# Kernel optimization log

Hardware: AMD Instinct MI355X
Metric: run time of the kernel (lower is better)

Reference implementation:

```python
import jax, jax.numpy as jnp
import numpy as np
from jax import lax

B, N, C = 8, 2000, 81            # batch, proposals, classes
MAX_INST = 100                    # config.detection_max_instances
MIN_CONF = 0.05                   # config.detection_min_confidence
NMS_THR = 0.3                     # config.detection_nms_threshold
H, W = 512, 512                   # config.image_shape[:2]
CLASS_OFFSET = 2.0                # > window extent, separates classes for batched NMS


def setup_inputs() -> dict:
    key = jax.random.key(0)
    k1, k2, k3, k4 = jax.random.split(key, 4)
    # valid normalized boxes (y1<y2, x1<x2)
    ctr = jax.random.uniform(k1, (B, N, 2))
    sz = jax.random.uniform(k2, (B, N, 2), minval=0.02, maxval=0.25)
    lo = jnp.clip(ctr - sz / 2, 0.0, 1.0)
    hi = jnp.clip(ctr + sz / 2, 0.0, 1.0)
    rois = jnp.stack([lo[..., 0], lo[..., 1], hi[..., 0], hi[..., 1]], axis=-1)
    probs = jax.nn.softmax(4.0 * jax.random.normal(k3, (B, N, C)), axis=-1)
    deltas = 0.1 * jax.random.normal(k4, (B, N, C, 4))
    bbox_std_dev = jnp.array([0.1, 0.1, 0.2, 0.2], jnp.float32)
    return {"rois": rois, "probs": probs, "deltas": deltas,
            "bbox_std_dev": bbox_std_dev}


def _apply_box_deltas(boxes, d):
    # boxes [N,4] (y1,x1,y2,x2), d [N,4] (dy,dx,log dh,log dw)
    h = boxes[:, 2] - boxes[:, 0]
    w = boxes[:, 3] - boxes[:, 1]
    cy = boxes[:, 0] + 0.5 * h + d[:, 0] * h
    cx = boxes[:, 1] + 0.5 * w + d[:, 1] * w
    h = h * jnp.exp(d[:, 2])
    w = w * jnp.exp(d[:, 3])
    return jnp.stack([cy - 0.5 * h, cx - 0.5 * w, cy + 0.5 * h, cx + 0.5 * w], axis=1)


def _pairwise_iou(b):
    # b [N,4] -> [N,N]
    area = (b[:, 2] - b[:, 0]) * (b[:, 3] - b[:, 1])
    yy1 = jnp.maximum(b[:, None, 0], b[None, :, 0])
    xx1 = jnp.maximum(b[:, None, 1], b[None, :, 1])
    yy2 = jnp.minimum(b[:, None, 2], b[None, :, 2])
    xx2 = jnp.minimum(b[:, None, 3], b[None, :, 3])
    inter = jnp.maximum(yy2 - yy1, 0.0) * jnp.maximum(xx2 - xx1, 0.0)
    union = area[:, None] + area[None, :] - inter
    return inter / jnp.maximum(union, 1e-12)


def _refine_one(rois, probs, deltas, bbox_std_dev):
    # rois [N,4], probs [N,C], deltas [N,C,4]
    cls = jnp.argmax(probs, axis=1)                       # [N] int
    idx = jnp.arange(N)
    scores = probs[idx, cls]                              # [N]
    d = deltas[idx, cls] * bbox_std_dev                   # [N,4]
    refined = jnp.clip(_apply_box_deltas(rois, d), 0.0, 1.0)  # window (0,0,1,1)
    valid = (cls > 0) & (scores >= MIN_CONF)
    # sort by score desc; invalid last
    order = jnp.argsort(-jnp.where(valid, scores, -jnp.inf))
    b = refined[order]
    s = scores[order]
    c = cls[order]
    v = valid[order]
    # per-class NMS via class-offset trick (equivalent to per-class NMS)
    ob = b + CLASS_OFFSET * c[:, None].astype(b.dtype)
    iou = _pairwise_iou(ob)                               # [N,N]

    def body(i, carry):
        keep, counts = carry
        sup = jnp.any(keep & (iou[i] > NMS_THR))
        ci = c[i]
        ok = v[i] & (~sup) & (counts[ci] < MAX_INST)      # per-class max_output_size
        return keep.at[i].set(ok), counts.at[ci].add(ok.astype(jnp.int32))

    keep, _ = lax.fori_loop(0, N, body,
                            (jnp.zeros((N,), bool), jnp.zeros((C,), jnp.int32)))
    kscores = jnp.where(keep, s, -jnp.inf)
    topv, topi = lax.top_k(kscores, MAX_INST)             # global top-k, sorted
    dvalid = topv > -jnp.inf
    boxes = jnp.where(dvalid[:, None], b[topi], 0.0)
    cls_f = jnp.where(dvalid, c[topi].astype(jnp.float32), 0.0)
    scr = jnp.where(dvalid, topv, 0.0)
    return jnp.concatenate([boxes, cls_f[:, None], scr[:, None]], axis=1)  # [MAX_INST,6]


def _attention_mask(det):
    # det [B,MAX_INST,6]; padded rows are all-zero boxes -> cover no pixels
    ys = (jnp.arange(H, dtype=jnp.float32) + 0.5) / H
    xs = (jnp.arange(W, dtype=jnp.float32) + 0.5) / W
    iny = (ys >= det[:, :, 0:1]) & (ys < det[:, :, 2:3])  # [B,D,H]
    inx = (xs >= det[:, :, 1:2]) & (xs < det[:, :, 3:4])  # [B,D,W]
    m = jnp.einsum('bdh,bdw->bhw', iny.astype(jnp.float32), inx.astype(jnp.float32))
    return (m > 0).astype(jnp.float32)


def reference(rois, probs, deltas, bbox_std_dev):
    det = jax.vmap(lambda r, p, dl: _refine_one(r, p, dl, bbox_std_dev))(rois, probs, deltas)
    mask = _attention_mask(det)
    return det, mask
```

## Files before the change

### kernel.cpp

```cpp
#include <hip/hip_runtime.h>
#include <math.h>

#define BB 8
#define NN 2000
#define CC 81
#define NPAD 2048
#define MAXI 100
#define HH 512
#define WW 512

__global__ void k_refine(const float* __restrict__ rois,
                         const float* __restrict__ probs,
                         const float* __restrict__ deltas,
                         const float* __restrict__ stdv,
                         float* __restrict__ score, int* __restrict__ cls,
                         int* __restrict__ valid, float* __restrict__ box,
                         unsigned long long* __restrict__ gkeys) {
#pragma clang fp contract(off)
  int g = blockIdx.x * 4 + (threadIdx.x >> 6);
  if (g >= BB * NPAD) return;
  int lane = threadIdx.x & 63;
  int b = g >> 11, n = g & (NPAD - 1);
  if (n >= NN) {
    if (lane == 0) {
      unsigned u = __float_as_uint(-INFINITY);
      u = ~u;
      gkeys[b * NPAD + n] =
          ((unsigned long long)u << 32) | (0xFFFFFFFFu - (unsigned)n);
      valid[b * NPAD + n] = 0;
    }
    return;
  }
  const float* pp = probs + ((size_t)b * NN + n) * CC;
  float best = -INFINITY;
  int bc = CC;
  for (int c = lane; c < CC; c += 64) {
    float p = pp[c];
    if (p > best) { best = p; bc = c; }
  }
  for (int off = 32; off; off >>= 1) {
    float ob = __shfl_xor(best, off, 64);
    int oc = __shfl_xor(bc, off, 64);
    if (ob > best || (ob == best && oc < bc)) { best = ob; bc = oc; }
  }
  if (lane == 0) {
    int idx = b * NPAD + n;
    const float* r = rois + ((size_t)b * NN + n) * 4;
    const float* dd = deltas + (((size_t)b * NN + n) * CC + bc) * 4;
    float d0 = dd[0] * stdv[0], d1 = dd[1] * stdv[1];
    float d2 = dd[2] * stdv[2], d3 = dd[3] * stdv[3];
    float y1 = r[0], x1 = r[1], y2 = r[2], x2 = r[3];
    float h = y2 - y1, w = x2 - x1;
    float cy = y1 + 0.5f * h + d0 * h;
    float cx = x1 + 0.5f * w + d1 * w;
    h = h * (float)exp((double)d2);
    w = w * (float)exp((double)d3);
    float ny1 = cy - 0.5f * h, nx1 = cx - 0.5f * w;
    float ny2 = cy + 0.5f * h, nx2 = cx + 0.5f * w;
    ny1 = fminf(fmaxf(ny1, 0.f), 1.f);
    nx1 = fminf(fmaxf(nx1, 0.f), 1.f);
    ny2 = fminf(fmaxf(ny2, 0.f), 1.f);
    nx2 = fminf(fmaxf(nx2, 0.f), 1.f);
    box[idx * 4 + 0] = ny1;
    box[idx * 4 + 1] = nx1;
    box[idx * 4 + 2] = ny2;
    box[idx * 4 + 3] = nx2;
    score[idx] = best;
    cls[idx] = bc;
    int v = (bc > 0 && best >= 0.05f) ? 1 : 0;
    valid[idx] = v;
    float ks = v ? best : -INFINITY;
    unsigned u = __float_as_uint(ks);
    u = (u & 0x80000000u) ? ~u : (u | 0x80000000u);
    gkeys[idx] = ((unsigned long long)u << 32) | (0xFFFFFFFFu - (unsigned)n);
  }
}

__global__ void k_rankp(const unsigned long long* __restrict__ gkeys,
                        int* __restrict__ partial) {
  __shared__ unsigned long long sk[256];
  int blk = blockIdx.x;
  int jp = blk & 7, ip = (blk >> 3) & 7, b = blk >> 6;
  int tid = threadIdx.x;
  sk[tid] = gkeys[b * NPAD + jp * 256 + tid];
  unsigned long long myk = gkeys[b * NPAD + ip * 256 + tid];
  __syncthreads();
  int cnt = 0;
#pragma unroll 8
  for (int j = 0; j < 256; j++) cnt += (sk[j] > myk) ? 1 : 0;
  partial[(b * 8 + jp) * NPAD + ip * 256 + tid] = cnt;
}

__global__ void k_perm(const int* __restrict__ partial, int* __restrict__ perm) {
  int t = blockIdx.x * 256 + threadIdx.x;
  int b = t >> 11, i = t & (NPAD - 1);
  int rank = 0;
#pragma unroll
  for (int jp = 0; jp < 8; jp++) rank += partial[(b * 8 + jp) * NPAD + i];
  perm[b * NPAD + rank] = i;
}

__global__ void k_nms(const float* __restrict__ score, const int* __restrict__ cls,
                      const int* __restrict__ valid, const float* __restrict__ box,
                      const int* __restrict__ perm, float* __restrict__ det) {
#pragma clang fp contract(off)
  int b = blockIdx.x, lane = threadIdx.x;
  int kept = 0;
  bool done = false;
  float k0y1 = 0.f, k0x1 = 0.f, k0y2 = 0.f, k0x2 = 0.f, k0a = 0.f;
  float k1y1 = 0.f, k1x1 = 0.f, k1y2 = 0.f, k1x2 = 0.f, k1a = 0.f;
  for (int base = 0; base < NN && !done; base += 64) {
    int pi = perm[b * NPAD + base + lane];
    int o = b * NPAD + pi;
    float4 bx = ((const float4*)box)[o];
    int lv = valid[o];
    int lc = cls[o];
    float lsc = score[o];
    int lim = (NN - base < 64) ? (NN - base) : 64;
    for (int j = 0; j < lim; j++) {
      int v = __shfl(lv, j, 64);
      if (!v) { done = true; break; }
      float y1 = __shfl(bx.x, j, 64);
      float x1 = __shfl(bx.y, j, 64);
      float y2 = __shfl(bx.z, j, 64);
      float x2 = __shfl(bx.w, j, 64);
      int c = __shfl(lc, j, 64);
      float off = 2.0f * (float)c;
      float oy1 = y1 + off, ox1 = x1 + off, oy2 = y2 + off, ox2 = x2 + off;
      float area_i = (oy2 - oy1) * (ox2 - ox1);
      bool pred = false;
      if (lane < kept) {
        float yy1 = fmaxf(oy1, k0y1), xx1 = fmaxf(ox1, k0x1);
        float yy2 = fminf(oy2, k0y2), xx2 = fminf(ox2, k0x2);
        float inter = fmaxf(yy2 - yy1, 0.f) * fmaxf(xx2 - xx1, 0.f);
        float uni = (area_i + k0a) - inter;
        pred = (inter / fmaxf(uni, 1e-12f)) > 0.3f;
      }
      if (64 + lane < kept) {
        float yy1 = fmaxf(oy1, k1y1), xx1 = fmaxf(ox1, k1x1);
        float yy2 = fminf(oy2, k1y2), xx2 = fminf(ox2, k1x2);
        float inter = fmaxf(yy2 - yy1, 0.f) * fmaxf(xx2 - xx1, 0.f);
        float uni = (area_i + k1a) - inter;
        pred = pred || ((inter / fmaxf(uni, 1e-12f)) > 0.3f);
      }
      if (__ballot(pred) == 0ULL) {
        if (kept < 64) {
          if (lane == kept) { k0y1 = oy1; k0x1 = ox1; k0y2 = oy2; k0x2 = ox2; k0a = area_i; }
        } else {
          if (lane == kept - 64) { k1y1 = oy1; k1x1 = ox1; k1y2 = oy2; k1x2 = ox2; k1a = area_i; }
        }
        float sc = __shfl(lsc, j, 64);
        if (lane == 0) {
          float* dr = det + ((size_t)b * MAXI + kept) * 6;
          dr[0] = y1; dr[1] = x1; dr[2] = y2; dr[3] = x2;
          dr[4] = (float)c; dr[5] = sc;
        }
        kept++;
        if (kept == MAXI) { done = true; break; }
      }
    }
  }
  int rem = (MAXI - kept) * 6;
  float* dr0 = det + ((size_t)b * MAXI + kept) * 6;
  for (int t = lane; t < rem; t += 64) dr0[t] = 0.f;
}

__global__ void k_mask(const float* __restrict__ det, float* __restrict__ mask) {
  __shared__ float lx1[MAXI], lx2[MAXI];
  __shared__ unsigned long long wmask[4];
  int x = blockIdx.x;
  int h = x & (HH - 1);
  int b = x >> 9;
  int tid = threadIdx.x;
  int wv = tid >> 6, ln = tid & 63;
  float ys = ((float)h + 0.5f) * (1.0f / 512.0f);
  bool inb = false;
  float bx1 = 0.f, bx2 = 0.f;
  if (tid < MAXI) {
    const float* dr = det + ((size_t)b * MAXI + tid) * 6;
    float y1 = dr[0], y2 = dr[2];
    bx1 = dr[1]; bx2 = dr[3];
    inb = (ys >= y1 && ys < y2);
  }
  unsigned long long bm = __ballot(inb);
  if (ln == 0) wmask[wv] = bm;
  __syncthreads();
  int n = __popcll(wmask[0]) + __popcll(wmask[1]);
  if (inb) {
    int pos = (wv ? __popcll(wmask[0]) : 0) +
              __popcll(bm & ((1ULL << ln) - 1ULL));
    lx1[pos] = bx1; lx2[pos] = bx2;
  }
  __syncthreads();
  float xs0 = ((float)tid + 0.5f) * (1.0f / 512.0f);
  float xs1 = ((float)(tid + 256) + 0.5f) * (1.0f / 512.0f);
  bool c0 = false, c1 = false;
  for (int t = 0; t < n; t++) {
    float a = lx1[t], bq = lx2[t];
    c0 = c0 || (xs0 >= a && xs0 < bq);
    c1 = c1 || (xs1 >= a && xs1 < bq);
  }
  float* row = mask + ((size_t)b * HH + h) * WW;
  row[tid] = c0 ? 1.0f : 0.0f;
  row[tid + 256] = c1 ? 1.0f : 0.0f;
}

extern "C" void kernel_launch(void* const* d_in, const int* in_sizes, int n_in,
                              void* d_out, int out_size, void* d_ws, size_t ws_size,
                              hipStream_t stream) {
  const float* rois = (const float*)d_in[0];
  const float* probs = (const float*)d_in[1];
  const float* deltas = (const float*)d_in[2];
  const float* stdv = (const float*)d_in[3];
  float* out = (float*)d_out;
  float* det = out;
  float* mask = out + BB * MAXI * 6;

  char* p = (char*)d_ws;
  unsigned long long* gkeys = (unsigned long long*)p; p += (size_t)BB * NPAD * 8;
  float* box     = (float*)p; p += (size_t)BB * NPAD * 16;
  float* score   = (float*)p; p += (size_t)BB * NPAD * 4;
  int*   cls     = (int*)p;   p += (size_t)BB * NPAD * 4;
  int*   valid   = (int*)p;   p += (size_t)BB * NPAD * 4;
  int*   partial = (int*)p;   p += (size_t)BB * 8 * NPAD * 4;
  int*   perm    = (int*)p;   p += (size_t)BB * NPAD * 4;

  k_refine<<<(BB * NPAD) / 4, 256, 0, stream>>>(rois, probs, deltas, stdv,
                                                score, cls, valid, box, gkeys);
  k_rankp<<<BB * 64, 256, 0, stream>>>(gkeys, partial);
  k_perm<<<BB * NPAD / 256, 256, 0, stream>>>(partial, perm);
  k_nms<<<BB, 64, 0, stream>>>(score, cls, valid, box, perm, det);
  k_mask<<<BB * HH, 256, 0, stream>>>(det, mask);
}
```

Before: 136.8 us.

## Fuse all five stages into one cooperative persistent kernel with grid syncs

Replaces the five separate launches (refine, partial rank, permutation, NMS, mask) with one cooperative kernel of 512 blocks that loops over each stage's work and uses grid.sync between stages. The aim is to remove per-launch overhead and the gaps between the small kernels. In exchange, the serial single-wave NMS stage now leaves the other blocks idle at a grid barrier, and each grid.sync carries its own cost.

```diff
diff --git a/kernel.cpp b/kernel.cpp
--- a/kernel.cpp
+++ b/kernel.cpp
@@ -1,5 +1,8 @@
 #include <hip/hip_runtime.h>
+#include <hip/hip_cooperative_groups.h>
 #include <math.h>
+
+namespace cg = cooperative_groups;
 
 #define BB 8
 #define NN 2000
@@ -9,200 +12,207 @@
 #define HH 512
 #define WW 512
 
-__global__ void k_refine(const float* __restrict__ rois,
-                         const float* __restrict__ probs,
-                         const float* __restrict__ deltas,
-                         const float* __restrict__ stdv,
-                         float* __restrict__ score, int* __restrict__ cls,
-                         int* __restrict__ valid, float* __restrict__ box,
-                         unsigned long long* __restrict__ gkeys) {
+__global__ void __launch_bounds__(256, 2)
+k_fused(const float* __restrict__ rois, const float* __restrict__ probs,
+        const float* __restrict__ deltas, const float* __restrict__ stdv,
+        float* __restrict__ score, int* __restrict__ cls,
+        int* __restrict__ valid, float* __restrict__ box,
+        unsigned long long* __restrict__ gkeys, int* __restrict__ partial,
+        int* __restrict__ perm, float* __restrict__ det,
+        float* __restrict__ mask) {
 #pragma clang fp contract(off)
-  int g = blockIdx.x * 4 + (threadIdx.x >> 6);
-  if (g >= BB * NPAD) return;
-  int lane = threadIdx.x & 63;
-  int b = g >> 11, n = g & (NPAD - 1);
-  if (n >= NN) {
-    if (lane == 0) {
-      unsigned u = __float_as_uint(-INFINITY);
-      u = ~u;
-      gkeys[b * NPAD + n] =
-          ((unsigned long long)u << 32) | (0xFFFFFFFFu - (unsigned)n);
-      valid[b * NPAD + n] = 0;
-    }
-    return;
-  }
-  const float* pp = probs + ((size_t)b * NN + n) * CC;
-  float best = -INFINITY;
-  int bc = CC;
-  for (int c = lane; c < CC; c += 64) {
-    float p = pp[c];
-    if (p > best) { best = p; bc = c; }
-  }
-  for (int off = 32; off; off >>= 1) {
-    float ob = __shfl_xor(best, off, 64);
-    int oc = __shfl_xor(bc, off, 64);
-    if (ob > best || (ob == best && oc < bc)) { best = ob; bc = oc; }
-  }
-  if (lane == 0) {
-    int idx = b * NPAD + n;
-    const float* r = rois + ((size_t)b * NN + n) * 4;
-    const float* dd = deltas + (((size_t)b * NN + n) * CC + bc) * 4;
-    float d0 = dd[0] * stdv[0], d1 = dd[1] * stdv[1];
-    float d2 = dd[2] * stdv[2], d3 = dd[3] * stdv[3];
-    float y1 = r[0], x1 = r[1], y2 = r[2], x2 = r[3];
-    float h = y2 - y1, w = x2 - x1;
-    float cy = y1 + 0.5f * h + d0 * h;
-    float cx = x1 + 0.5f * w + d1 * w;
-    h = h * (float)exp((double)d2);
-    w = w * (float)exp((double)d3);
-    float ny1 = cy - 0.5f * h, nx1 = cx - 0.5f * w;
-    float ny2 = cy + 0.5f * h, nx2 = cx + 0.5f * w;
-    ny1 = fminf(fmaxf(ny1, 0.f), 1.f);
-    nx1 = fminf(fmaxf(nx1, 0.f), 1.f);
-    ny2 = fminf(fmaxf(ny2, 0.f), 1.f);
-    nx2 = fminf(fmaxf(nx2, 0.f), 1.f);
-    box[idx * 4 + 0] = ny1;
-    box[idx * 4 + 1] = nx1;
-    box[idx * 4 + 2] = ny2;
-    box[idx * 4 + 3] = nx2;
-    score[idx] = best;
-    cls[idx] = bc;
-    int v = (bc > 0 && best >= 0.05f) ? 1 : 0;
-    valid[idx] = v;
-    float ks = v ? best : -INFINITY;
-    unsigned u = __float_as_uint(ks);
-    u = (u & 0x80000000u) ? ~u : (u | 0x80000000u);
-    gkeys[idx] = ((unsigned long long)u << 32) | (0xFFFFFFFFu - (unsigned)n);
-  }
-}
-
-__global__ void k_rankp(const unsigned long long* __restrict__ gkeys,
-                        int* __restrict__ partial) {
   __shared__ unsigned long long sk[256];
-  int blk = blockIdx.x;
-  int jp = blk & 7, ip = (blk >> 3) & 7, b = blk >> 6;
-  int tid = threadIdx.x;
-  sk[tid] = gkeys[b * NPAD + jp * 256 + tid];
-  unsigned long long myk = gkeys[b * NPAD + ip * 256 + tid];
-  __syncthreads();
-  int cnt = 0;
-#pragma unroll 8
-  for (int j = 0; j < 256; j++) cnt += (sk[j] > myk) ? 1 : 0;
-  partial[(b * 8 + jp) * NPAD + ip * 256 + tid] = cnt;
-}
-
-__global__ void k_perm(const int* __restrict__ partial, int* __restrict__ perm) {
-  int t = blockIdx.x * 256 + threadIdx.x;
-  int b = t >> 11, i = t & (NPAD - 1);
-  int rank = 0;
-#pragma unroll
-  for (int jp = 0; jp < 8; jp++) rank += partial[(b * 8 + jp) * NPAD + i];
-  perm[b * NPAD + rank] = i;
-}
-
-__global__ void k_nms(const float* __restrict__ score, const int* __restrict__ cls,
-                      const int* __restrict__ valid, const float* __restrict__ box,
-                      const int* __restrict__ perm, float* __restrict__ det) {
-#pragma clang fp contract(off)
-  int b = blockIdx.x, lane = threadIdx.x;
-  int kept = 0;
-  bool done = false;
-  float k0y1 = 0.f, k0x1 = 0.f, k0y2 = 0.f, k0x2 = 0.f, k0a = 0.f;
-  float k1y1 = 0.f, k1x1 = 0.f, k1y2 = 0.f, k1x2 = 0.f, k1a = 0.f;
-  for (int base = 0; base < NN && !done; base += 64) {
-    int pi = perm[b * NPAD + base + lane];
-    int o = b * NPAD + pi;
-    float4 bx = ((const float4*)box)[o];
-    int lv = valid[o];
-    int lc = cls[o];
-    float lsc = score[o];
-    int lim = (NN - base < 64) ? (NN - base) : 64;
-    for (int j = 0; j < lim; j++) {
-      int v = __shfl(lv, j, 64);
-      if (!v) { done = true; break; }
-      float y1 = __shfl(bx.x, j, 64);
-      float x1 = __shfl(bx.y, j, 64);
-      float y2 = __shfl(bx.z, j, 64);
-      float x2 = __shfl(bx.w, j, 64);
-      int c = __shfl(lc, j, 64);
-      float off = 2.0f * (float)c;
-      float oy1 = y1 + off, ox1 = x1 + off, oy2 = y2 + off, ox2 = x2 + off;
-      float area_i = (oy2 - oy1) * (ox2 - ox1);
-      bool pred = false;
-      if (lane < kept) {
-        float yy1 = fmaxf(oy1, k0y1), xx1 = fmaxf(ox1, k0x1);
-        float yy2 = fminf(oy2, k0y2), xx2 = fminf(ox2, k0x2);
-        float inter = fmaxf(yy2 - yy1, 0.f) * fmaxf(xx2 - xx1, 0.f);
-        float uni = (area_i + k0a) - inter;
-        pred = (inter / fmaxf(uni, 1e-12f)) > 0.3f;
-      }
-      if (64 + lane < kept) {
-        float yy1 = fmaxf(oy1, k1y1), xx1 = fmaxf(ox1, k1x1);
-        float yy2 = fminf(oy2, k1y2), xx2 = fminf(ox2, k1x2);
-        float inter = fmaxf(yy2 - yy1, 0.f) * fmaxf(xx2 - xx1, 0.f);
-        float uni = (area_i + k1a) - inter;
-        pred = pred || ((inter / fmaxf(uni, 1e-12f)) > 0.3f);
-      }
-      if (__ballot(pred) == 0ULL) {
-        if (kept < 64) {
-          if (lane == kept) { k0y1 = oy1; k0x1 = ox1; k0y2 = oy2; k0x2 = ox2; k0a = area_i; }
-        } else {
-          if (lane == kept - 64) { k1y1 = oy1; k1x1 = ox1; k1y2 = oy2; k1x2 = ox2; k1a = area_i; }
-        }
-        float sc = __shfl(lsc, j, 64);
-        if (lane == 0) {
-          float* dr = det + ((size_t)b * MAXI + kept) * 6;
-          dr[0] = y1; dr[1] = x1; dr[2] = y2; dr[3] = x2;
-          dr[4] = (float)c; dr[5] = sc;
-        }
-        kept++;
-        if (kept == MAXI) { done = true; break; }
-      }
-    }
-  }
-  int rem = (MAXI - kept) * 6;
-  float* dr0 = det + ((size_t)b * MAXI + kept) * 6;
-  for (int t = lane; t < rem; t += 64) dr0[t] = 0.f;
-}
-
-__global__ void k_mask(const float* __restrict__ det, float* __restrict__ mask) {
   __shared__ float lx1[MAXI], lx2[MAXI];
   __shared__ unsigned long long wmask[4];
-  int x = blockIdx.x;
-  int h = x & (HH - 1);
-  int b = x >> 9;
+  cg::grid_group grid = cg::this_grid();
   int tid = threadIdx.x;
-  int wv = tid >> 6, ln = tid & 63;
-  float ys = ((float)h + 0.5f) * (1.0f / 512.0f);
-  bool inb = false;
-  float bx1 = 0.f, bx2 = 0.f;
-  if (tid < MAXI) {
-    const float* dr = det + ((size_t)b * MAXI + tid) * 6;
-    float y1 = dr[0], y2 = dr[2];
-    bx1 = dr[1]; bx2 = dr[3];
-    inb = (ys >= y1 && ys < y2);
-  }
-  unsigned long long bm = __ballot(inb);
-  if (ln == 0) wmask[wv] = bm;
-  __syncthreads();
-  int n = __popcll(wmask[0]) + __popcll(wmask[1]);
-  if (inb) {
-    int pos = (wv ? __popcll(wmask[0]) : 0) +
-              __popcll(bm & ((1ULL << ln) - 1ULL));
-    lx1[pos] = bx1; lx2[pos] = bx2;
-  }
-  __syncthreads();
-  float xs0 = ((float)tid + 0.5f) * (1.0f / 512.0f);
-  float xs1 = ((float)(tid + 256) + 0.5f) * (1.0f / 512.0f);
-  bool c0 = false, c1 = false;
-  for (int t = 0; t < n; t++) {
-    float a = lx1[t], bq = lx2[t];
-    c0 = c0 || (xs0 >= a && xs0 < bq);
-    c1 = c1 || (xs1 >= a && xs1 < bq);
-  }
-  float* row = mask + ((size_t)b * HH + h) * WW;
-  row[tid] = c0 ? 1.0f : 0.0f;
-  row[tid + 256] = c1 ? 1.0f : 0.0f;
+  int lane = tid & 63;
+  int wv = tid >> 6;
+
+  {
+    int wave = blockIdx.x * 4 + wv;
+    for (int it = 0; it < 8; ++it) {
+      int g = wave + 2048 * it;
+      int b = g >> 11, n = g & (NPAD - 1);
+      if (n >= NN) {
+        if (lane == 0) {
+          unsigned u = __float_as_uint(-INFINITY);
+          u = ~u;
+          gkeys[b * NPAD + n] =
+              ((unsigned long long)u << 32) | (0xFFFFFFFFu - (unsigned)n);
+          valid[b * NPAD + n] = 0;
+        }
+        continue;
+      }
+      const float* pp = probs + ((size_t)b * NN + n) * CC;
+      float best = -INFINITY;
+      int bc = CC;
+      for (int c = lane; c < CC; c += 64) {
+        float p = pp[c];
+        if (p > best) { best = p; bc = c; }
+      }
+      for (int off = 32; off; off >>= 1) {
+        float ob = __shfl_xor(best, off, 64);
+        int oc = __shfl_xor(bc, off, 64);
+        if (ob > best || (ob == best && oc < bc)) { best = ob; bc = oc; }
+      }
+      if (lane == 0) {
+        int idx = b * NPAD + n;
+        const float* r = rois + ((size_t)b * NN + n) * 4;
+        const float* dd = deltas + (((size_t)b * NN + n) * CC + bc) * 4;
+        float d0 = dd[0] * stdv[0], d1 = dd[1] * stdv[1];
+        float d2 = dd[2] * stdv[2], d3 = dd[3] * stdv[3];
+        float y1 = r[0], x1 = r[1], y2 = r[2], x2 = r[3];
+        float h = y2 - y1, w = x2 - x1;
+        float cy = y1 + 0.5f * h + d0 * h;
+        float cx = x1 + 0.5f * w + d1 * w;
+        h = h * (float)exp((double)d2);
+        w = w * (float)exp((double)d3);
+        float ny1 = cy - 0.5f * h, nx1 = cx - 0.5f * w;
+        float ny2 = cy + 0.5f * h, nx2 = cx + 0.5f * w;
+        ny1 = fminf(fmaxf(ny1, 0.f), 1.f);
+        nx1 = fminf(fmaxf(nx1, 0.f), 1.f);
+        ny2 = fminf(fmaxf(ny2, 0.f), 1.f);
+        nx2 = fminf(fmaxf(nx2, 0.f), 1.f);
+        box[idx * 4 + 0] = ny1;
+        box[idx * 4 + 1] = nx1;
+        box[idx * 4 + 2] = ny2;
+        box[idx * 4 + 3] = nx2;
+        score[idx] = best;
+        cls[idx] = bc;
+        int v = (bc > 0 && best >= 0.05f) ? 1 : 0;
+        valid[idx] = v;
+        float ks = v ? best : -INFINITY;
+        unsigned u = __float_as_uint(ks);
+        u = (u & 0x80000000u) ? ~u : (u | 0x80000000u);
+        gkeys[idx] = ((unsigned long long)u << 32) | (0xFFFFFFFFu - (unsigned)n);
+      }
+    }
+  }
+  grid.sync();
+
+  {
+    int blk = blockIdx.x;
+    int jp = blk & 7, ip = (blk >> 3) & 7, b = blk >> 6;
+    sk[tid] = gkeys[b * NPAD + jp * 256 + tid];
+    unsigned long long myk = gkeys[b * NPAD + ip * 256 + tid];
+    __syncthreads();
+    int cnt = 0;
+#pragma unroll 8
+    for (int j = 0; j < 256; j++) cnt += (sk[j] > myk) ? 1 : 0;
+    partial[(b * 8 + jp) * NPAD + ip * 256 + tid] = cnt;
+  }
+  grid.sync();
+
+  if (blockIdx.x < 64) {
+    int t = blockIdx.x * 256 + tid;
+    int b = t >> 11, i = t & (NPAD - 1);
+    int rank = 0;
+#pragma unroll
+    for (int jp = 0; jp < 8; jp++) rank += partial[(b * 8 + jp) * NPAD + i];
+    perm[b * NPAD + rank] = i;
+  }
+  grid.sync();
+
+  if (blockIdx.x < BB && tid < 64) {
+    int b = blockIdx.x;
+    int kept = 0;
+    bool done = false;
+    float k0y1 = 0.f, k0x1 = 0.f, k0y2 = 0.f, k0x2 = 0.f, k0a = 0.f;
+    float k1y1 = 0.f, k1x1 = 0.f, k1y2 = 0.f, k1x2 = 0.f, k1a = 0.f;
+    for (int base = 0; base < NN && !done; base += 64) {
+      int pi = perm[b * NPAD + base + lane];
+      int o = b * NPAD + pi;
+      float4 bx = ((const float4*)box)[o];
+      int lv = valid[o];
+      int lc = cls[o];
+      float lsc = score[o];
+      int lim = (NN - base < 64) ? (NN - base) : 64;
+      for (int j = 0; j < lim; j++) {
+        int v = __shfl(lv, j, 64);
+        if (!v) { done = true; break; }
+        float y1 = __shfl(bx.x, j, 64);
+        float x1 = __shfl(bx.y, j, 64);
+        float y2 = __shfl(bx.z, j, 64);
+        float x2 = __shfl(bx.w, j, 64);
+        int c = __shfl(lc, j, 64);
+        float off = 2.0f * (float)c;
+        float oy1 = y1 + off, ox1 = x1 + off, oy2 = y2 + off, ox2 = x2 + off;
+        float area_i = (oy2 - oy1) * (ox2 - ox1);
+        bool pred = false;
+        if (lane < kept) {
+          float yy1 = fmaxf(oy1, k0y1), xx1 = fmaxf(ox1, k0x1);
+          float yy2 = fminf(oy2, k0y2), xx2 = fminf(ox2, k0x2);
+          float inter = fmaxf(yy2 - yy1, 0.f) * fmaxf(xx2 - xx1, 0.f);
+          float uni = (area_i + k0a) - inter;
+          pred = (inter / fmaxf(uni, 1e-12f)) > 0.3f;
+        }
+        if (64 + lane < kept) {
+          float yy1 = fmaxf(oy1, k1y1), xx1 = fmaxf(ox1, k1x1);
+          float yy2 = fminf(oy2, k1y2), xx2 = fminf(ox2, k1x2);
+          float inter = fmaxf(yy2 - yy1, 0.f) * fmaxf(xx2 - xx1, 0.f);
+          float uni = (area_i + k1a) - inter;
+          pred = pred || ((inter / fmaxf(uni, 1e-12f)) > 0.3f);
+        }
+        if (__ballot(pred) == 0ULL) {
+          if (kept < 64) {
+            if (lane == kept) { k0y1 = oy1; k0x1 = ox1; k0y2 = oy2; k0x2 = ox2; k0a = area_i; }
+          } else {
+            if (lane == kept - 64) { k1y1 = oy1; k1x1 = ox1; k1y2 = oy2; k1x2 = ox2; k1a = area_i; }
+          }
+          float sc = __shfl(lsc, j, 64);
+          if (lane == 0) {
+            float* dr = det + ((size_t)b * MAXI + kept) * 6;
+            dr[0] = y1; dr[1] = x1; dr[2] = y2; dr[3] = x2;
+            dr[4] = (float)c; dr[5] = sc;
+          }
+          kept++;
+          if (kept == MAXI) { done = true; break; }
+        }
+      }
+    }
+    int rem = (MAXI - kept) * 6;
+    float* dr0 = det + ((size_t)b * MAXI + kept) * 6;
+    for (int t = lane; t < rem; t += 64) dr0[t] = 0.f;
+  }
+  grid.sync();
+
+  for (int it = 0; it < 8; ++it) {
+    int row = blockIdx.x + 512 * it;
+    int h = row & (HH - 1);
+    int b = row >> 9;
+    __syncthreads();
+    float ys = ((float)h + 0.5f) * (1.0f / 512.0f);
+    bool inb = false;
+    float bx1 = 0.f, bx2 = 0.f;
+    if (tid < MAXI) {
+      const float* dr = det + ((size_t)b * MAXI + tid) * 6;
+      float y1 = dr[0], y2 = dr[2];
+      bx1 = dr[1]; bx2 = dr[3];
+      inb = (ys >= y1 && ys < y2);
+    }
+    unsigned long long bm = __ballot(inb);
+    if (lane == 0) wmask[wv] = bm;
+    __syncthreads();
+    int n = __popcll(wmask[0]) + __popcll(wmask[1]);
+    if (inb) {
+      int pos = (wv ? __popcll(wmask[0]) : 0) +
+                __popcll(bm & ((1ULL << lane) - 1ULL));
+      lx1[pos] = bx1; lx2[pos] = bx2;
+    }
+    __syncthreads();
+    float xs0 = ((float)tid + 0.5f) * (1.0f / 512.0f);
+    float xs1 = ((float)(tid + 256) + 0.5f) * (1.0f / 512.0f);
+    bool c0 = false, c1 = false;
+    for (int t = 0; t < n; t++) {
+      float a = lx1[t], bq = lx2[t];
+      c0 = c0 || (xs0 >= a && xs0 < bq);
+      c1 = c1 || (xs1 >= a && xs1 < bq);
+    }
+    float* rowp = mask + ((size_t)b * HH + h) * WW;
+    rowp[tid] = c0 ? 1.0f : 0.0f;
+    rowp[tid + 256] = c1 ? 1.0f : 0.0f;
+  }
 }
 
 extern "C" void kernel_launch(void* const* d_in, const int* in_sizes, int n_in,
@@ -225,10 +235,8 @@
   int*   partial = (int*)p;   p += (size_t)BB * 8 * NPAD * 4;
   int*   perm    = (int*)p;   p += (size_t)BB * NPAD * 4;
 
-  k_refine<<<(BB * NPAD) / 4, 256, 0, stream>>>(rois, probs, deltas, stdv,
-                                                score, cls, valid, box, gkeys);
-  k_rankp<<<BB * 64, 256, 0, stream>>>(gkeys, partial);
-  k_perm<<<BB * NPAD / 256, 256, 0, stream>>>(partial, perm);
-  k_nms<<<BB, 64, 0, stream>>>(score, cls, valid, box, perm, det);
-  k_mask<<<BB * HH, 256, 0, stream>>>(det, mask);
+  void* args[] = {&rois, &probs, &deltas, &stdv, &score, &cls, &valid,
+                  &box, &gkeys, &partial, &perm, &det, &mask};
+  hipLaunchCooperativeKernel((const void*)k_fused, dim3(512), dim3(256),
+                             args, 0, stream);
 }
```

Measured after the change: 347.6 us. 2.54x slower.

## Fuse ranking sort and NMS into one kernel with shared-memory bitonic sort

Applied to the files above, without the earlier changes.

Replaces the two-kernel rank-count sort (partial counts plus permutation scatter) and the separate NMS kernel with one kernel per image. That kernel bitonic-sorts the 2048 packed keys in shared memory with 1024 threads, then runs NMS on a single wavefront, decoding proposal indices straight from the sorted keys. This drops two kernel launches and the global partial/perm round trips. The cost is only 8 blocks doing the sort, with 66 barrier stages each.

```diff
diff --git a/kernel.cpp b/kernel.cpp
--- a/kernel.cpp
+++ b/kernel.cpp
@@ -76,41 +76,39 @@
   }
 }
 
-__global__ void k_rankp(const unsigned long long* __restrict__ gkeys,
-                        int* __restrict__ partial) {
-  __shared__ unsigned long long sk[256];
-  int blk = blockIdx.x;
-  int jp = blk & 7, ip = (blk >> 3) & 7, b = blk >> 6;
-  int tid = threadIdx.x;
-  sk[tid] = gkeys[b * NPAD + jp * 256 + tid];
-  unsigned long long myk = gkeys[b * NPAD + ip * 256 + tid];
+__global__ void __launch_bounds__(1024)
+k_sortnms(const unsigned long long* __restrict__ gkeys,
+          const float* __restrict__ score, const int* __restrict__ cls,
+          const int* __restrict__ valid, const float* __restrict__ box,
+          float* __restrict__ det) {
+#pragma clang fp contract(off)
+  __shared__ unsigned long long skey[NPAD];
+  int b = blockIdx.x, tid = threadIdx.x;
+  skey[tid] = gkeys[b * NPAD + tid];
+  skey[tid + 1024] = gkeys[b * NPAD + tid + 1024];
+  for (unsigned k = 2; k <= NPAD; k <<= 1) {
+    for (unsigned j = k >> 1; j > 0; j >>= 1) {
+      __syncthreads();
+      unsigned i = tid;
+      for (int rep = 0; rep < 2; rep++, i += 1024) {
+        unsigned l = i ^ j;
+        if (l > i) {
+          unsigned long long a = skey[i], c = skey[l];
+          bool desc = ((i & k) == 0);
+          if (desc ? (a < c) : (a > c)) { skey[i] = c; skey[l] = a; }
+        }
+      }
+    }
+  }
   __syncthreads();
-  int cnt = 0;
-#pragma unroll 8
-  for (int j = 0; j < 256; j++) cnt += (sk[j] > myk) ? 1 : 0;
-  partial[(b * 8 + jp) * NPAD + ip * 256 + tid] = cnt;
-}
-
-__global__ void k_perm(const int* __restrict__ partial, int* __restrict__ perm) {
-  int t = blockIdx.x * 256 + threadIdx.x;
-  int b = t >> 11, i = t & (NPAD - 1);
-  int rank = 0;
-#pragma unroll
-  for (int jp = 0; jp < 8; jp++) rank += partial[(b * 8 + jp) * NPAD + i];
-  perm[b * NPAD + rank] = i;
-}
-
-__global__ void k_nms(const float* __restrict__ score, const int* __restrict__ cls,
-                      const int* __restrict__ valid, const float* __restrict__ box,
-                      const int* __restrict__ perm, float* __restrict__ det) {
-#pragma clang fp contract(off)
-  int b = blockIdx.x, lane = threadIdx.x;
+  if (tid >= 64) return;
+  int lane = tid;
   int kept = 0;
   bool done = false;
   float k0y1 = 0.f, k0x1 = 0.f, k0y2 = 0.f, k0x2 = 0.f, k0a = 0.f;
   float k1y1 = 0.f, k1x1 = 0.f, k1y2 = 0.f, k1x2 = 0.f, k1a = 0.f;
   for (int base = 0; base < NN && !done; base += 64) {
-    int pi = perm[b * NPAD + base + lane];
+    int pi = (int)(0xFFFFFFFFu - (unsigned)(skey[base + lane] & 0xFFFFFFFFu));
     int o = b * NPAD + pi;
     float4 bx = ((const float4*)box)[o];
     int lv = valid[o];
@@ -222,13 +220,9 @@
   float* score   = (float*)p; p += (size_t)BB * NPAD * 4;
   int*   cls     = (int*)p;   p += (size_t)BB * NPAD * 4;
   int*   valid   = (int*)p;   p += (size_t)BB * NPAD * 4;
-  int*   partial = (int*)p;   p += (size_t)BB * 8 * NPAD * 4;
-  int*   perm    = (int*)p;   p += (size_t)BB * NPAD * 4;
 
   k_refine<<<(BB * NPAD) / 4, 256, 0, stream>>>(rois, probs, deltas, stdv,
                                                 score, cls, valid, box, gkeys);
-  k_rankp<<<BB * 64, 256, 0, stream>>>(gkeys, partial);
-  k_perm<<<BB * NPAD / 256, 256, 0, stream>>>(partial, perm);
-  k_nms<<<BB, 64, 0, stream>>>(score, cls, valid, box, perm, det);
+  k_sortnms<<<BB, 1024, 0, stream>>>(gkeys, score, cls, valid, box, det);
   k_mask<<<BB * HH, 256, 0, stream>>>(det, mask);
 }
```

After: 151.7 us. 1.11x slower.
